# Performance work log

Hardware: AMD Instinct MI355X
Metric: run time of the kernel (lower is better)

The kernel has to match this reference:

```python
import jax, jax.numpy as jnp
import numpy as np

# Module hyper-parameters (match init_kwargs)
H = 8          # num_heads
F = 32         # attention_filters
HF = H * F     # 256, equals input channels C
RY, RX = 2, 2  # spatial_radius
PH, PW = 2 * RY + 1, 2 * RX + 1
S = PH * PW    # 25 neighbor offsets


def setup_inputs() -> dict:
    key = jax.random.key(0)
    ks = jax.random.split(key, 6)
    B, Y, X, C = 8, 128, 128, 256
    x = jax.random.normal(ks[0], (B, Y, X, C), dtype=jnp.float32)
    sc = 0.02
    Wq = jax.random.normal(ks[1], (C, HF), dtype=jnp.float32) * sc
    Wk = jax.random.normal(ks[2], (C, HF), dtype=jnp.float32) * sc
    Wv = jax.random.normal(ks[3], (C, HF), dtype=jnp.float32) * sc
    Wout = jax.random.normal(ks[4], (HF, C), dtype=jnp.float32) * sc
    pos_emb = jax.random.normal(ks[5], (S, HF), dtype=jnp.float32) * sc
    return {"x": x, "Wq": Wq, "Wk": Wk, "Wv": Wv, "Wout": Wout, "pos_emb": pos_emb}


def _centers(n, r):
    # clipped patch-center coordinate for each position
    c = jnp.arange(n)
    return jnp.clip(c, r, n - r - 1)


def reference(x, Wq, Wk, Wv, Wout, pos_emb):
    B, Y, X, C = x.shape
    dtype = x.dtype
    # 1x1 conv projections == channel matmuls
    Q = jnp.einsum('byxc,cf->byxf', x, Wq)
    K = jnp.einsum('byxc,cf->byxf', x, Wk)
    V = jnp.einsum('byxc,cf->byxf', x, Wv)

    # query spatial positional embedding (relative position to clipped center)
    yc = _centers(Y, RY)
    xc = _centers(X, RX)
    y_rel = jnp.arange(Y) - yc + RY          # [Y]
    x_rel = jnp.arange(X) - xc + RX          # [X]
    q_idx = y_rel[:, None] * PW + x_rel[None, :]  # [Y, X]
    Q = Q + pos_emb[q_idx]                   # [B,Y,X,HF]
    Q = Q.reshape(B, Y, X, H, F)

    scale = jnp.asarray(1.0 / np.sqrt(F), dtype)

    offsets = [(dy, dx) for dy in range(-RY, RY + 1) for dx in range(-RX, RX + 1)]

    # pass 1: per-offset scores (loop over fixed 25-neighborhood, rest vectorized)
    scores = []
    for s_idx, (dy, dx) in enumerate(offsets):
        ny = jnp.clip(yc + dy, 0, Y - 1)     # [Y]
        nx = jnp.clip(xc + dx, 0, X - 1)     # [X]
        Kn = K[:, ny][:, :, nx] + pos_emb[s_idx]        # [B,Y,X,HF]
        Kn = Kn.reshape(B, Y, X, H, F)
        scores.append(jnp.einsum('byxhf,byxhf->byxh', Q, Kn) * scale)
    scores = jnp.stack(scores, axis=-1)      # [B,Y,X,H,S]
    weights = jax.nn.softmax(scores, axis=-1)

    # pass 2: weighted value accumulation
    out_acc = jnp.zeros((B, Y, X, H, F), dtype=dtype)
    for s_idx, (dy, dx) in enumerate(offsets):
        ny = jnp.clip(yc + dy, 0, Y - 1)
        nx = jnp.clip(xc + dx, 0, X - 1)
        Vn = V[:, ny][:, :, nx].reshape(B, Y, X, H, F)
        out_acc = out_acc + weights[..., s_idx, None] * Vn

    out_acc = out_acc.reshape(B, Y, X, HF)
    out = jnp.einsum('byxf,fc->byxc', out_acc, Wout)
    return out
```

## Files before the change

kernel.cpp:

```cpp
#include <hip/hip_runtime.h>

#define DEVI __device__ __forceinline__

typedef short v8s __attribute__((ext_vector_type(8)));
typedef float v4f __attribute__((ext_vector_type(4)));
typedef unsigned short u16;

typedef __attribute__((address_space(3))) unsigned int lds_u32;
typedef const __attribute__((address_space(1))) unsigned int glb_u32;

DEVI float bf2f(short s) {
  union { unsigned u; float f; } cv;
  cv.u = ((unsigned)(u16)s) << 16;
  return cv.f;
}
DEVI short f2bf(float f) {
  union { float f; unsigned u; } cv; cv.f = f;
  unsigned u = cv.u;
  return (short)((u + 0x7FFFu + ((u >> 16) & 1u)) >> 16);
}
DEVI void gld16(const void* g, void* l) {
  __builtin_amdgcn_global_load_lds((glb_u32*)g, (lds_u32*)l, 16, 0, 0);
}

__global__ void prep_weights(const float* __restrict__ Wq, const float* __restrict__ Wk,
                             const float* __restrict__ Wv, const float* __restrict__ Wout,
                             short* __restrict__ WcT, short* __restrict__ WoT) {
  int n = blockIdx.x;
  int k = threadIdx.x;
  float v;
  if (n < 256)      v = Wq[k * 256 + n];
  else if (n < 512) v = Wk[k * 256 + (n - 256)];
  else              v = Wv[k * 256 + (n - 512)];
  WcT[n * 256 + k] = f2bf(v);
  if (n < 256) WoT[n * 256 + k] = f2bf(Wout[k * 256 + n]);
}

__global__ void x_cast(const float* __restrict__ x, short* __restrict__ xb) {
  for (size_t gidx = (size_t)blockIdx.x * 256 + threadIdx.x; gidx < 4194304;
       gidx += (size_t)4096 * 256) {
    const float4* src = reinterpret_cast<const float4*>(x + gidx * 8);
    float4 a = src[0], c = src[1];
    v8s pk;
    pk[0] = f2bf(a.x); pk[1] = f2bf(a.y); pk[2] = f2bf(a.z); pk[3] = f2bf(a.w);
    pk[4] = f2bf(c.x); pk[5] = f2bf(c.y); pk[6] = f2bf(c.z); pk[7] = f2bf(c.w);
    *reinterpret_cast<v8s*>(xb + gidx * 8) = pk;
  }
}

__launch_bounds__(256, 3)
__global__ void proj_gemm(const short* __restrict__ xb, const short* __restrict__ WcT,
                          const float* __restrict__ pos_emb,
                          short* __restrict__ Qb, short* __restrict__ Kb,
                          short* __restrict__ Vb) {
  __shared__ short As[128 * 64];
  __shared__ short Bs[128 * 64];
  const int t = threadIdx.x;
  const int bi = blockIdx.x;
  const int xcd = bi & 7;
  const int j = bi >> 3;
  const int mgl = j / 6, nt = j % 6;
  const int mtg = xcd * 32 + mgl;
  const int m0 = mtg * 512;
  const int n0 = nt * 128;
  const int wave = t >> 6, lane = t & 63;
  const int wm = (wave & 1) * 64, wn = (wave >> 1) * 64;
  const int lr = lane & 15, g = lane >> 4;

  const int ro = lane >> 3;
  const int colb = ((lane & 7) * 16) ^ (ro << 4);
  const char* aSrc0 = reinterpret_cast<const char*>(xb + (size_t)(m0 + ro) * 256) + colb;
  const char* bSrc  = reinterpret_cast<const char*>(WcT + (size_t)(n0 + ro) * 256) + colb;

#pragma unroll 1
  for (int u = 0; u < 4; ++u) {
    const char* aSrc = aSrc0 + (size_t)u * 128 * 512;

    v4f acc[4][4];
#pragma unroll
    for (int i = 0; i < 4; ++i)
#pragma unroll
      for (int jj = 0; jj < 4; ++jj) acc[i][jj] = (v4f){0.f, 0.f, 0.f, 0.f};

#pragma unroll 1
    for (int ks = 0; ks < 4; ++ks) {
      __syncthreads();
#pragma unroll
      for (int c = 0; c < 4; ++c) {
        int cc = wave * 4 + c;
        gld16(aSrc + (size_t)cc * 8 * 512 + ks * 128, (char*)As + cc * 1024);
        gld16(bSrc + (size_t)cc * 8 * 512 + ks * 128, (char*)Bs + cc * 1024);
      }
      __syncthreads();
#pragma unroll
      for (int kk = 0; kk < 2; ++kk) {
        v8s af[4], bfr[4];
#pragma unroll
        for (int i = 0; i < 4; ++i) {
          int row = wm + i * 16 + lr;
          int byte = (row * 128 + kk * 64 + g * 16) ^ ((row & 7) << 4);
          af[i] = *reinterpret_cast<const v8s*>(reinterpret_cast<const char*>(As) + byte);
        }
#pragma unroll
        for (int jj = 0; jj < 4; ++jj) {
          int rn = wn + jj * 16 + lr;
          int byte = (rn * 128 + kk * 64 + g * 16) ^ ((rn & 7) << 4);
          bfr[jj] = *reinterpret_cast<const v8s*>(reinterpret_cast<const char*>(Bs) + byte);
        }
#pragma unroll
        for (int i = 0; i < 4; ++i)
#pragma unroll
          for (int jj = 0; jj < 4; ++jj)
            acc[i][jj] = __builtin_amdgcn_mfma_f32_16x16x32_bf16(af[i], bfr[jj], acc[i][jj], 0, 0, 0);
      }
    }

#pragma unroll
    for (int i = 0; i < 4; ++i) {
#pragma unroll
      for (int jj = 0; jj < 4; ++jj) {
        int colg = n0 + wn + jj * 16 + lr;
#pragma unroll
        for (int r = 0; r < 4; ++r) {
          int p = m0 + u * 128 + wm + i * 16 + g * 4 + r;
          float v = acc[i][jj][r];
          if (nt < 2) {
            int yy = (p >> 7) & 127, xx = p & 127;
            int qi = (yy - min(max(yy, 2), 125) + 2) * 5 + (xx - min(max(xx, 2), 125) + 2);
            v += pos_emb[qi * 256 + colg];
            Qb[(size_t)p * 256 + colg] = f2bf(v);
          } else if (nt < 4) {
            Kb[(size_t)p * 256 + (colg - 256)] = f2bf(v);
          } else {
            Vb[(size_t)p * 256 + (colg - 512)] = f2bf(v);
          }
        }
      }
    }
  }
}

__launch_bounds__(256, 4)
__global__ void attn_kernel(const short* __restrict__ Qb, const short* __restrict__ Kb,
                            const short* __restrict__ Vb, const float* __restrict__ pos_emb,
                            short* __restrict__ ACC) {
  __shared__ float pe[25 * 256];
  for (int i = threadIdx.x; i < 1600; i += 256) {
    float4 vv = reinterpret_cast<const float4*>(pos_emb)[i];
    int w = i * 4;
    int f = w & 255;
    int dst = (w & ~255) + (f ^ ((f >> 5) << 2));
    *reinterpret_cast<float4*>(pe + dst) = vv;
  }

  const int t = threadIdx.x;
  const int half = t & 1, h = (t >> 1) & 7, pl = t >> 4;
  const int id = blockIdx.x;
  const int b = id & 7;
  const int local = id >> 3;
  const int bx = local & 31, by = local >> 5;
  const int xx = bx * 4 + (pl & 3);
  const int yy = by * 4 + (pl >> 2);
  const int yc = min(max(yy, 2), 125), xc = min(max(xx, 2), 125);
  const int fo = h * 32 + half * 16;
  const int hx4 = h << 2;
  const size_t pbase = ((size_t)((b * 128 + yy) * 128 + xx)) * 256 + fo;
  const size_t cbase = ((size_t)((b * 128 + yc) * 128 + xc)) * 256 + fo;
  const float SCALE = 0.17677669529663689f;

  float q[16];
  {
    v8s q0 = *reinterpret_cast<const v8s*>(Qb + pbase);
    v8s q1 = *reinterpret_cast<const v8s*>(Qb + pbase + 8);
#pragma unroll
    for (int e = 0; e < 8; ++e) { q[e] = bf2f(q0[e]); q[8 + e] = bf2f(q1[e]); }
  }
  __syncthreads();

  float l = 0.f;
  float oa[16];
#pragma unroll
  for (int f = 0; f < 16; ++f) oa[f] = 0.f;

  const short* kb = Kb + cbase;
  const short* vb = Vb + cbase;
  const float* pb = pe + h * 32;
  const int j0 = (half * 16) ^ hx4;
  const int j1 = (half * 16 + 4) ^ hx4;
  const int j2 = (half * 16 + 8) ^ hx4;
  const int j3 = (half * 16 + 12) ^ hx4;

#pragma unroll 1
  for (int dy = -2; dy <= 2; ++dy) {
    const short* krow = kb + dy * (128 * 256);
    const short* vrow = vb + dy * (128 * 256);
    const float* prow = pb + ((dy + 2) * 5) * 256;
#pragma unroll 1
    for (int dx = -2; dx <= 2; ++dx) {
      const short* kp = krow + dx * 256;
      const short* vp = vrow + dx * 256;
      const float* pp = prow + (dx + 2) * 256;
      v8s k0 = *reinterpret_cast<const v8s*>(kp);
      v8s k1 = *reinterpret_cast<const v8s*>(kp + 8);
      v8s v0 = *reinterpret_cast<const v8s*>(vp);
      v8s v1 = *reinterpret_cast<const v8s*>(vp + 8);
      float4 p0 = *reinterpret_cast<const float4*>(pp + j0);
      float4 p1 = *reinterpret_cast<const float4*>(pp + j1);
      float4 p2 = *reinterpret_cast<const float4*>(pp + j2);
      float4 p3 = *reinterpret_cast<const float4*>(pp + j3);
      float d0 = 0.f, d1 = 0.f, d2 = 0.f, d3 = 0.f;
#pragma unroll
      for (int e = 0; e < 4; ++e) {
        d0 = fmaf(q[e], bf2f(k0[e]), d0);
        d1 = fmaf(q[4 + e], bf2f(k0[4 + e]), d1);
        d2 = fmaf(q[8 + e], bf2f(k1[e]), d2);
        d3 = fmaf(q[12 + e], bf2f(k1[4 + e]), d3);
      }
      d0 = fmaf(q[0], p0.x, d0); d0 = fmaf(q[1], p0.y, d0);
      d0 = fmaf(q[2], p0.z, d0); d0 = fmaf(q[3], p0.w, d0);
      d1 = fmaf(q[4], p1.x, d1); d1 = fmaf(q[5], p1.y, d1);
      d1 = fmaf(q[6], p1.z, d1); d1 = fmaf(q[7], p1.w, d1);
      d2 = fmaf(q[8], p2.x, d2); d2 = fmaf(q[9], p2.y, d2);
      d2 = fmaf(q[10], p2.z, d2); d2 = fmaf(q[11], p2.w, d2);
      d3 = fmaf(q[12], p3.x, d3); d3 = fmaf(q[13], p3.y, d3);
      d3 = fmaf(q[14], p3.z, d3); d3 = fmaf(q[15], p3.w, d3);
      float part = ((d0 + d1) + (d2 + d3)) * SCALE;
      float full = part + __shfl_xor(part, 1);
      float w = __expf(full);
      l += w;
#pragma unroll
      for (int e = 0; e < 8; ++e) oa[e] = fmaf(w, bf2f(v0[e]), oa[e]);
#pragma unroll
      for (int e = 0; e < 8; ++e) oa[8 + e] = fmaf(w, bf2f(v1[e]), oa[8 + e]);
    }
  }

  float inv = 1.f / l;
  v8s o0, o1;
#pragma unroll
  for (int e = 0; e < 8; ++e) { o0[e] = f2bf(oa[e] * inv); o1[e] = f2bf(oa[8 + e] * inv); }
  *reinterpret_cast<v8s*>(ACC + pbase) = o0;
  *reinterpret_cast<v8s*>(ACC + pbase + 8) = o1;
}

__launch_bounds__(256, 3)
__global__ void out_gemm(const short* __restrict__ A, const short* __restrict__ WoT,
                         float* __restrict__ out) {
  __shared__ short As[128 * 64];
  __shared__ short Bs[128 * 64];
  const int t = threadIdx.x;
  const int bi = blockIdx.x;
  const int xcd = bi & 7;
  const int j = bi >> 3;
  const int mgl = j / 2, nt = j % 2;
  const int mtg = xcd * 64 + mgl;
  const int m0 = mtg * 256;
  const int n0 = nt * 128;
  const int wave = t >> 6, lane = t & 63;
  const int wm = (wave & 1) * 64, wn = (wave >> 1) * 64;
  const int lr = lane & 15, g = lane >> 4;

  const int ro = lane >> 3;
  const int colb = ((lane & 7) * 16) ^ (ro << 4);
  const char* aSrc0 = reinterpret_cast<const char*>(A + (size_t)(m0 + ro) * 256) + colb;
  const char* bSrc  = reinterpret_cast<const char*>(WoT + (size_t)(n0 + ro) * 256) + colb;

#pragma unroll 1
  for (int u = 0; u < 2; ++u) {
    const char* aSrc = aSrc0 + (size_t)u * 128 * 512;

    v4f acc[4][4];
#pragma unroll
    for (int i = 0; i < 4; ++i)
#pragma unroll
      for (int jj = 0; jj < 4; ++jj) acc[i][jj] = (v4f){0.f, 0.f, 0.f, 0.f};

#pragma unroll 1
    for (int ks = 0; ks < 4; ++ks) {
      __syncthreads();
#pragma unroll
      for (int c = 0; c < 4; ++c) {
        int cc = wave * 4 + c;
        gld16(aSrc + (size_t)cc * 8 * 512 + ks * 128, (char*)As + cc * 1024);
        gld16(bSrc + (size_t)cc * 8 * 512 + ks * 128, (char*)Bs + cc * 1024);
      }
      __syncthreads();
#pragma unroll
      for (int kk = 0; kk < 2; ++kk) {
        v8s af[4], bfr[4];
#pragma unroll
        for (int i = 0; i < 4; ++i) {
          int row = wm + i * 16 + lr;
          int byte = (row * 128 + kk * 64 + g * 16) ^ ((row & 7) << 4);
          af[i] = *reinterpret_cast<const v8s*>(reinterpret_cast<const char*>(As) + byte);
        }
#pragma unroll
        for (int jj = 0; jj < 4; ++jj) {
          int rn = wn + jj * 16 + lr;
          int byte = (rn * 128 + kk * 64 + g * 16) ^ ((rn & 7) << 4);
          bfr[jj] = *reinterpret_cast<const v8s*>(reinterpret_cast<const char*>(Bs) + byte);
        }
#pragma unroll
        for (int i = 0; i < 4; ++i)
#pragma unroll
          for (int jj = 0; jj < 4; ++jj)
            acc[i][jj] = __builtin_amdgcn_mfma_f32_16x16x32_bf16(af[i], bfr[jj], acc[i][jj], 0, 0, 0);
      }
    }

#pragma unroll
    for (int i = 0; i < 4; ++i) {
#pragma unroll
      for (int jj = 0; jj < 4; ++jj) {
        int colg = n0 + wn + jj * 16 + lr;
#pragma unroll
        for (int r = 0; r < 4; ++r) {
          int p = m0 + u * 128 + wm + i * 16 + g * 4 + r;
          out[(size_t)p * 256 + colg] = acc[i][jj][r];
        }
      }
    }
  }
}

extern "C" void kernel_launch(void* const* d_in, const int* in_sizes, int n_in,
                              void* d_out, int out_size, void* d_ws, size_t ws_size,
                              hipStream_t stream) {
  const float* x       = (const float*)d_in[0];
  const float* Wq      = (const float*)d_in[1];
  const float* Wk      = (const float*)d_in[2];
  const float* Wv      = (const float*)d_in[3];
  const float* Wout    = (const float*)d_in[4];
  const float* pos_emb = (const float*)d_in[5];
  float* out = (float*)d_out;

  char* ws = (char*)d_ws;
  short* WcT  = (short*)ws;
  short* WoT  = (short*)(ws + 393216);
  short* Qb   = (short*)(ws + 524288);
  short* Kb   = Qb + (size_t)131072 * 256;
  short* Vb   = Kb + (size_t)131072 * 256;
  short* ACCb = Vb + (size_t)131072 * 256;
  short* xb   = ACCb;

  prep_weights<<<768, 256, 0, stream>>>(Wq, Wk, Wv, Wout, WcT, WoT);
  x_cast<<<4096, 256, 0, stream>>>(x, xb);
  proj_gemm<<<1536, 256, 0, stream>>>(xb, WcT, pos_emb, Qb, Kb, Vb);
  attn_kernel<<<8192, 256, 0, stream>>>(Qb, Kb, Vb, pos_emb, ACCb);
  out_gemm<<<1024, 256, 0, stream>>>(ACCb, WoT, out);
}
```

Baseline: 377.5 us.

## Double-buffer LDS tiles in projection and output GEMMs to overlap loads

Both GEMM kernels now use two LDS buffers and issue the next K-step's global-to-LDS loads before computing the current one. The u/ks nested loops are flattened into one stage loop, with epilogue stores every fourth step and manual vmcnt waits plus barriers. This hides global load latency behind MFMA work. In exchange, LDS per block doubles and launch bounds drop from 3 to 2 blocks per CU, which lowers occupancy. Stores at the end of each tile also sit inside the pipelined loop.

```diff
diff --git a/kernel.cpp b/kernel.cpp
--- a/kernel.cpp
+++ b/kernel.cpp
@@ -48,13 +48,13 @@
   }
 }
 
-__launch_bounds__(256, 3)
+__launch_bounds__(256, 2)
 __global__ void proj_gemm(const short* __restrict__ xb, const short* __restrict__ WcT,
                           const float* __restrict__ pos_emb,
                           short* __restrict__ Qb, short* __restrict__ Kb,
                           short* __restrict__ Vb) {
-  __shared__ short As[128 * 64];
-  __shared__ short Bs[128 * 64];
+  __shared__ short As[2][128 * 64];
+  __shared__ short Bs[2][128 * 64];
   const int t = threadIdx.x;
   const int bi = blockIdx.x;
   const int xcd = bi & 7;
@@ -70,73 +70,92 @@
   const int ro = lane >> 3;
   const int colb = ((lane & 7) * 16) ^ (ro << 4);
   const char* aSrc0 = reinterpret_cast<const char*>(xb + (size_t)(m0 + ro) * 256) + colb;
-  const char* bSrc  = reinterpret_cast<const char*>(WcT + (size_t)(n0 + ro) * 256) + colb;
-
+  const char* bSrc0 = reinterpret_cast<const char*>(WcT + (size_t)(n0 + ro) * 256) + colb;
+
+  v4f acc[4][4];
+#pragma unroll
+  for (int i = 0; i < 4; ++i)
+#pragma unroll
+    for (int jj = 0; jj < 4; ++jj) acc[i][jj] = (v4f){0.f, 0.f, 0.f, 0.f};
+
+  auto stage = [&](int buf, int s) {
+    const int u = s >> 2, ks = s & 3;
+    const char* aS = aSrc0 + (size_t)u * 128 * 512 + ks * 128;
+    const char* bS = bSrc0 + ks * 128;
+    char* aD = (char*)As + buf * 16384;
+    char* bD = (char*)Bs + buf * 16384;
+#pragma unroll
+    for (int c = 0; c < 4; ++c) {
+      int cc = wave * 4 + c;
+      gld16(aS + (size_t)cc * 8 * 512, aD + cc * 1024);
+      gld16(bS + (size_t)cc * 8 * 512, bD + cc * 1024);
+    }
+  };
+
+  stage(0, 0);
 #pragma unroll 1
-  for (int u = 0; u < 4; ++u) {
-    const char* aSrc = aSrc0 + (size_t)u * 128 * 512;
-
-    v4f acc[4][4];
-#pragma unroll
-    for (int i = 0; i < 4; ++i)
-#pragma unroll
-      for (int jj = 0; jj < 4; ++jj) acc[i][jj] = (v4f){0.f, 0.f, 0.f, 0.f};
-
-#pragma unroll 1
-    for (int ks = 0; ks < 4; ++ks) {
-      __syncthreads();
-#pragma unroll
-      for (int c = 0; c < 4; ++c) {
-        int cc = wave * 4 + c;
-        gld16(aSrc + (size_t)cc * 8 * 512 + ks * 128, (char*)As + cc * 1024);
-        gld16(bSrc + (size_t)cc * 8 * 512 + ks * 128, (char*)Bs + cc * 1024);
-      }
-      __syncthreads();
-#pragma unroll
-      for (int kk = 0; kk < 2; ++kk) {
-        v8s af[4], bfr[4];
-#pragma unroll
-        for (int i = 0; i < 4; ++i) {
-          int row = wm + i * 16 + lr;
-          int byte = (row * 128 + kk * 64 + g * 16) ^ ((row & 7) << 4);
-          af[i] = *reinterpret_cast<const v8s*>(reinterpret_cast<const char*>(As) + byte);
-        }
+  for (int s = 0; s < 16; ++s) {
+    const int buf = s & 1;
+    if (s < 15) {
+      stage(buf ^ 1, s + 1);
+      asm volatile("s_waitcnt vmcnt(8)" ::: "memory");
+    } else {
+      asm volatile("s_waitcnt vmcnt(0)" ::: "memory");
+    }
+    __builtin_amdgcn_s_barrier();
+    __builtin_amdgcn_sched_barrier(0);
+
+    const char* aB = (const char*)As + buf * 16384;
+    const char* bB = (const char*)Bs + buf * 16384;
+#pragma unroll
+    for (int kk = 0; kk < 2; ++kk) {
+      v8s af[4], bfr[4];
+#pragma unroll
+      for (int i = 0; i < 4; ++i) {
+        int row = wm + i * 16 + lr;
+        int byte = (row * 128 + kk * 64 + g * 16) ^ ((row & 7) << 4);
+        af[i] = *reinterpret_cast<const v8s*>(aB + byte);
+      }
+#pragma unroll
+      for (int jj = 0; jj < 4; ++jj) {
+        int rn = wn + jj * 16 + lr;
+        int byte = (rn * 128 + kk * 64 + g * 16) ^ ((rn & 7) << 4);
+        bfr[jj] = *reinterpret_cast<const v8s*>(bB + byte);
+      }
+#pragma unroll
+      for (int i = 0; i < 4; ++i)
+#pragma unroll
+        for (int jj = 0; jj < 4; ++jj)
+          acc[i][jj] = __builtin_amdgcn_mfma_f32_16x16x32_bf16(af[i], bfr[jj], acc[i][jj], 0, 0, 0);
+    }
+
+    if ((s & 3) == 3) {
+      const int u = s >> 2;
+#pragma unroll
+      for (int i = 0; i < 4; ++i) {
 #pragma unroll
         for (int jj = 0; jj < 4; ++jj) {
-          int rn = wn + jj * 16 + lr;
-          int byte = (rn * 128 + kk * 64 + g * 16) ^ ((rn & 7) << 4);
-          bfr[jj] = *reinterpret_cast<const v8s*>(reinterpret_cast<const char*>(Bs) + byte);
-        }
-#pragma unroll
-        for (int i = 0; i < 4; ++i)
-#pragma unroll
-          for (int jj = 0; jj < 4; ++jj)
-            acc[i][jj] = __builtin_amdgcn_mfma_f32_16x16x32_bf16(af[i], bfr[jj], acc[i][jj], 0, 0, 0);
-      }
-    }
-
-#pragma unroll
-    for (int i = 0; i < 4; ++i) {
-#pragma unroll
-      for (int jj = 0; jj < 4; ++jj) {
-        int colg = n0 + wn + jj * 16 + lr;
-#pragma unroll
-        for (int r = 0; r < 4; ++r) {
-          int p = m0 + u * 128 + wm + i * 16 + g * 4 + r;
-          float v = acc[i][jj][r];
-          if (nt < 2) {
-            int yy = (p >> 7) & 127, xx = p & 127;
-            int qi = (yy - min(max(yy, 2), 125) + 2) * 5 + (xx - min(max(xx, 2), 125) + 2);
-            v += pos_emb[qi * 256 + colg];
-            Qb[(size_t)p * 256 + colg] = f2bf(v);
-          } else if (nt < 4) {
-            Kb[(size_t)p * 256 + (colg - 256)] = f2bf(v);
-          } else {
-            Vb[(size_t)p * 256 + (colg - 512)] = f2bf(v);
+          int colg = n0 + wn + jj * 16 + lr;
+#pragma unroll
+          for (int r = 0; r < 4; ++r) {
+            int p = m0 + u * 128 + wm + i * 16 + g * 4 + r;
+            float v = acc[i][jj][r];
+            if (nt < 2) {
+              int yy = (p >> 7) & 127, xx = p & 127;
+              int qi = (yy - min(max(yy, 2), 125) + 2) * 5 + (xx - min(max(xx, 2), 125) + 2);
+              v += pos_emb[qi * 256 + colg];
+              Qb[(size_t)p * 256 + colg] = f2bf(v);
+            } else if (nt < 4) {
+              Kb[(size_t)p * 256 + (colg - 256)] = f2bf(v);
+            } else {
+              Vb[(size_t)p * 256 + (colg - 512)] = f2bf(v);
+            }
+            acc[i][jj][r] = 0.f;
           }
         }
       }
     }
+    __builtin_amdgcn_s_barrier();
   }
 }
 
@@ -243,11 +262,11 @@
   *reinterpret_cast<v8s*>(ACC + pbase + 8) = o1;
 }
 
-__launch_bounds__(256, 3)
+__launch_bounds__(256, 2)
 __global__ void out_gemm(const short* __restrict__ A, const short* __restrict__ WoT,
                          float* __restrict__ out) {
-  __shared__ short As[128 * 64];
-  __shared__ short Bs[128 * 64];
+  __shared__ short As[2][128 * 64];
+  __shared__ short Bs[2][128 * 64];
   const int t = threadIdx.x;
   const int bi = blockIdx.x;
   const int xcd = bi & 7;
@@ -263,63 +282,82 @@
   const int ro = lane >> 3;
   const int colb = ((lane & 7) * 16) ^ (ro << 4);
   const char* aSrc0 = reinterpret_cast<const char*>(A + (size_t)(m0 + ro) * 256) + colb;
-  const char* bSrc  = reinterpret_cast<const char*>(WoT + (size_t)(n0 + ro) * 256) + colb;
-
+  const char* bSrc0 = reinterpret_cast<const char*>(WoT + (size_t)(n0 + ro) * 256) + colb;
+
+  v4f acc[4][4];
+#pragma unroll
+  for (int i = 0; i < 4; ++i)
+#pragma unroll
+    for (int jj = 0; jj < 4; ++jj) acc[i][jj] = (v4f){0.f, 0.f, 0.f, 0.f};
+
+  auto stage = [&](int buf, int s) {
+    const int u = s >> 2, ks = s & 3;
+    const char* aS = aSrc0 + (size_t)u * 128 * 512 + ks * 128;
+    const char* bS = bSrc0 + ks * 128;
+    char* aD = (char*)As + buf * 16384;
+    char* bD = (char*)Bs + buf * 16384;
+#pragma unroll
+    for (int c = 0; c < 4; ++c) {
+      int cc = wave * 4 + c;
+      gld16(aS + (size_t)cc * 8 * 512, aD + cc * 1024);
+      gld16(bS + (size_t)cc * 8 * 512, bD + cc * 1024);
+    }
+  };
+
+  stage(0, 0);
 #pragma unroll 1
-  for (int u = 0; u < 2; ++u) {
-    const char* aSrc = aSrc0 + (size_t)u * 128 * 512;
-
-    v4f acc[4][4];
-#pragma unroll
-    for (int i = 0; i < 4; ++i)
-#pragma unroll
-      for (int jj = 0; jj < 4; ++jj) acc[i][jj] = (v4f){0.f, 0.f, 0.f, 0.f};
-
-#pragma unroll 1
-    for (int ks = 0; ks < 4; ++ks) {
-      __syncthreads();
-#pragma unroll
-      for (int c = 0; c < 4; ++c) {
-        int cc = wave * 4 + c;
-        gld16(aSrc + (size_t)cc * 8 * 512 + ks * 128, (char*)As + cc * 1024);
-        gld16(bSrc + (size_t)cc * 8 * 512 + ks * 128, (char*)Bs + cc * 1024);
-      }
-      __syncthreads();
-#pragma unroll
-      for (int kk = 0; kk < 2; ++kk) {
-        v8s af[4], bfr[4];
-#pragma unroll
-        for (int i = 0; i < 4; ++i) {
-          int row = wm + i * 16 + lr;
-          int byte = (row * 128 + kk * 64 + g * 16) ^ ((row & 7) << 4);
-          af[i] = *reinterpret_cast<const v8s*>(reinterpret_cast<const char*>(As) + byte);
+  for (int s = 0; s < 8; ++s) {
+    const int buf = s & 1;
+    if (s < 7) {
+      stage(buf ^ 1, s + 1);
+      asm volatile("s_waitcnt vmcnt(8)" ::: "memory");
+    } else {
+      asm volatile("s_waitcnt vmcnt(0)" ::: "memory");
+    }
+    __builtin_amdgcn_s_barrier();
+    __builtin_amdgcn_sched_barrier(0);
+
+    const char* aB = (const char*)As + buf * 16384;
+    const char* bB = (const char*)Bs + buf * 16384;
+#pragma unroll
+    for (int kk = 0; kk < 2; ++kk) {
+      v8s af[4], bfr[4];
+#pragma unroll
+      for (int i = 0; i < 4; ++i) {
+        int row = wm + i * 16 + lr;
+        int byte = (row * 128 + kk * 64 + g * 16) ^ ((row & 7) << 4);
+        af[i] = *reinterpret_cast<const v8s*>(aB + byte);
+      }
+#pragma unroll
+      for (int jj = 0; jj < 4; ++jj) {
+        int rn = wn + jj * 16 + lr;
+        int byte = (rn * 128 + kk * 64 + g * 16) ^ ((rn & 7) << 4);
+        bfr[jj] = *reinterpret_cast<const v8s*>(bB + byte);
+      }
+#pragma unroll
+      for (int i = 0; i < 4; ++i)
+#pragma unroll
+        for (int jj = 0; jj < 4; ++jj)
+          acc[i][jj] = __builtin_amdgcn_mfma_f32_16x16x32_bf16(af[i], bfr[jj], acc[i][jj], 0, 0, 0);
+    }
+
+    if ((s & 3) == 3) {
+      const int u = s >> 2;
+#pragma unroll
+      for (int i = 0; i < 4; ++i) {
+#pragma unroll
+        for (int jj = 0; jj < 4; ++jj) {
+          int colg = n0 + wn + jj * 16 + lr;
+#pragma unroll
+          for (int r = 0; r < 4; ++r) {
+            int p = m0 + u * 128 + wm + i * 16 + g * 4 + r;
+            out[(size_t)p * 256 + colg] = acc[i][jj][r];
+            acc[i][jj][r] = 0.f;
+          }
         }
-#pragma unroll
-        for (int jj = 0; jj < 4; ++jj) {
-          int rn = wn + jj * 16 + lr;
-          int byte = (rn * 128 + kk * 64 + g * 16) ^ ((rn & 7) << 4);
-          bfr[jj] = *reinterpret_cast<const v8s*>(reinterpret_cast<const char*>(Bs) + byte);
-        }
-#pragma unroll
-        for (int i = 0; i < 4; ++i)
-#pragma unroll
-          for (int jj = 0; jj < 4; ++jj)
-            acc[i][jj] = __builtin_amdgcn_mfma_f32_16x16x32_bf16(af[i], bfr[jj], acc[i][jj], 0, 0, 0);
-      }
-    }
-
-#pragma unroll
-    for (int i = 0; i < 4; ++i) {
-#pragma unroll
-      for (int jj = 0; jj < 4; ++jj) {
-        int colg = n0 + wn + jj * 16 + lr;
-#pragma unroll
-        for (int r = 0; r < 4; ++r) {
-          int p = m0 + u * 128 + wm + i * 16 + g * 4 + r;
-          out[(size_t)p * 256 + colg] = acc[i][jj][r];
-        }
-      }
-    }
+      }
+    }
+    __builtin_amdgcn_s_barrier();
   }
 }
 
```

Result: slower. 409.4 us (+8.4%).

## Triple-buffer projection GEMM loads and stage epilogue through LDS for vector stores

Applied to the files above, without the earlier changes.

Restructures the QKV projection GEMM into one flattened 32-step loop with a triple-buffered LDS ring, using BK=32 slices. Global-to-LDS loads are issued two steps ahead, with explicit vmcnt waits and raw barriers in place of __syncthreads. The epilogue now writes accumulators as bf16 into LDS, then reads them back row-contiguous and emits 16-byte vector stores, adding pos_emb for Q in that pass. This aims to hide load latency and replace scattered 2-byte global stores with coalesced ones. The cost is more barriers and an extra bf16 rounding of Q before the pos_emb add.

```diff
diff --git a/kernel.cpp b/kernel.cpp
--- a/kernel.cpp
+++ b/kernel.cpp
@@ -22,6 +22,9 @@
 DEVI void gld16(const void* g, void* l) {
   __builtin_amdgcn_global_load_lds((glb_u32*)g, (lds_u32*)l, 16, 0, 0);
 }
+#define SBAR() __builtin_amdgcn_s_barrier()
+#define SCHED0() __builtin_amdgcn_sched_barrier(0)
+#define LGKM0() asm volatile("s_waitcnt lgkmcnt(0)" ::: "memory")
 
 __global__ void prep_weights(const float* __restrict__ Wq, const float* __restrict__ Wk,
                              const float* __restrict__ Wv, const float* __restrict__ Wout,
@@ -53,8 +56,7 @@
                           const float* __restrict__ pos_emb,
                           short* __restrict__ Qb, short* __restrict__ Kb,
                           short* __restrict__ Vb) {
-  __shared__ short As[128 * 64];
-  __shared__ short Bs[128 * 64];
+  __shared__ short L[3][8192];
   const int t = threadIdx.x;
   const int bi = blockIdx.x;
   const int xcd = bi & 7;
@@ -67,76 +69,121 @@
   const int wm = (wave & 1) * 64, wn = (wave >> 1) * 64;
   const int lr = lane & 15, g = lane >> 4;
 
-  const int ro = lane >> 3;
-  const int colb = ((lane & 7) * 16) ^ (ro << 4);
-  const char* aSrc0 = reinterpret_cast<const char*>(xb + (size_t)(m0 + ro) * 256) + colb;
-  const char* bSrc  = reinterpret_cast<const char*>(WcT + (size_t)(n0 + ro) * 256) + colb;
-
-#pragma unroll 1
-  for (int u = 0; u < 4; ++u) {
-    const char* aSrc = aSrc0 + (size_t)u * 128 * 512;
-
-    v4f acc[4][4];
+  const int srow = wave * 16 + (lane >> 2);
+  const int scu = (lane & 3) ^ ((lane >> 2) & 3);
+  const char* aSrcBase = reinterpret_cast<const char*>(xb) + (size_t)(m0 + srow) * 512 + scu * 16;
+  const char* bSrcBase = reinterpret_cast<const char*>(WcT) + (size_t)(n0 + srow) * 512 + scu * 16;
+
+  v4f acc[4][4];
+#pragma unroll
+  for (int i = 0; i < 4; ++i)
+#pragma unroll
+    for (int jj = 0; jj < 4; ++jj) acc[i][jj] = (v4f){0.f, 0.f, 0.f, 0.f};
+
+  auto stage = [&](int buf, int s) {
+    const int um = s >> 3, ks = s & 7;
+    const char* aS = aSrcBase + (size_t)um * 65536 + ks * 64;
+    const char* bS = bSrcBase + ks * 64;
+    char* aD = (char*)&L[buf][0] + wave * 1024;
+    char* bD = (char*)&L[buf][4096] + wave * 1024;
+    gld16(aS, aD);
+    gld16(aS + 32768, aD + 4096);
+    gld16(bS, bD);
+    gld16(bS + 32768, bD + 4096);
+  };
+
+  stage(0, 0);
+  stage(1, 1);
+
+#pragma unroll 1
+  for (int s = 0; s < 32; ++s) {
+    const int buf = s % 3;
+    if (s < 30) stage((s + 2) % 3, s + 2);
+    if (s >= 30) {
+      if (s == 30) asm volatile("s_waitcnt vmcnt(4)" ::: "memory");
+      else         asm volatile("s_waitcnt vmcnt(0)" ::: "memory");
+    } else if (s > 0 && (s & 7) == 0) {
+      if (nt < 2) asm volatile("s_waitcnt vmcnt(32)" ::: "memory");
+      else        asm volatile("s_waitcnt vmcnt(16)" ::: "memory");
+    } else {
+      asm volatile("s_waitcnt vmcnt(8)" ::: "memory");
+    }
+    SBAR();
+    SCHED0();
+
+    const char* aB = (const char*)&L[buf][0];
+    const char* bB = (const char*)&L[buf][4096];
+    v8s af[4], bfr[4];
+#pragma unroll
+    for (int i = 0; i < 4; ++i) {
+      int row = wm + i * 16 + lr;
+      af[i] = *reinterpret_cast<const v8s*>(aB + row * 64 + ((g * 16) ^ ((row & 3) << 4)));
+    }
+#pragma unroll
+    for (int jj = 0; jj < 4; ++jj) {
+      int rn = wn + jj * 16 + lr;
+      bfr[jj] = *reinterpret_cast<const v8s*>(bB + rn * 64 + ((g * 16) ^ ((rn & 3) << 4)));
+    }
 #pragma unroll
     for (int i = 0; i < 4; ++i)
 #pragma unroll
-      for (int jj = 0; jj < 4; ++jj) acc[i][jj] = (v4f){0.f, 0.f, 0.f, 0.f};
-
-#pragma unroll 1
-    for (int ks = 0; ks < 4; ++ks) {
-      __syncthreads();
-#pragma unroll
-      for (int c = 0; c < 4; ++c) {
-        int cc = wave * 4 + c;
-        gld16(aSrc + (size_t)cc * 8 * 512 + ks * 128, (char*)As + cc * 1024);
-        gld16(bSrc + (size_t)cc * 8 * 512 + ks * 128, (char*)Bs + cc * 1024);
-      }
-      __syncthreads();
-#pragma unroll
-      for (int kk = 0; kk < 2; ++kk) {
-        v8s af[4], bfr[4];
-#pragma unroll
-        for (int i = 0; i < 4; ++i) {
-          int row = wm + i * 16 + lr;
-          int byte = (row * 128 + kk * 64 + g * 16) ^ ((row & 7) << 4);
-          af[i] = *reinterpret_cast<const v8s*>(reinterpret_cast<const char*>(As) + byte);
-        }
-#pragma unroll
-        for (int jj = 0; jj < 4; ++jj) {
-          int rn = wn + jj * 16 + lr;
-          int byte = (rn * 128 + kk * 64 + g * 16) ^ ((rn & 7) << 4);
-          bfr[jj] = *reinterpret_cast<const v8s*>(reinterpret_cast<const char*>(Bs) + byte);
-        }
-#pragma unroll
-        for (int i = 0; i < 4; ++i)
-#pragma unroll
-          for (int jj = 0; jj < 4; ++jj)
-            acc[i][jj] = __builtin_amdgcn_mfma_f32_16x16x32_bf16(af[i], bfr[jj], acc[i][jj], 0, 0, 0);
-      }
-    }
-
-#pragma unroll
-    for (int i = 0; i < 4; ++i) {
-#pragma unroll
-      for (int jj = 0; jj < 4; ++jj) {
-        int colg = n0 + wn + jj * 16 + lr;
-#pragma unroll
-        for (int r = 0; r < 4; ++r) {
-          int p = m0 + u * 128 + wm + i * 16 + g * 4 + r;
-          float v = acc[i][jj][r];
+      for (int jj = 0; jj < 4; ++jj)
+        acc[i][jj] = __builtin_amdgcn_mfma_f32_16x16x32_bf16(af[i], bfr[jj], acc[i][jj], 0, 0, 0);
+
+    if ((s & 7) == 7) {
+      const int um = s >> 3;
+      char* tb = (char*)&L[buf][0];
+#pragma unroll 1
+      for (int pass = 0; pass < 2; ++pass) {
+        LGKM0(); SBAR(); SCHED0();
+        if (wm == pass * 64) {
+#pragma unroll
+          for (int i = 0; i < 4; ++i)
+#pragma unroll
+            for (int jj = 0; jj < 4; ++jj)
+#pragma unroll
+              for (int r = 0; r < 4; ++r) {
+                int rowl = i * 16 + g * 4 + r;
+                int col = wn + jj * 16 + lr;
+                int byte = (rowl * 256 + col * 2) ^ ((rowl & 7) << 4);
+                *reinterpret_cast<short*>(tb + byte) = f2bf(acc[i][jj][r]);
+              }
+        }
+        LGKM0(); SBAR(); SCHED0();
+        {
+          int row = t >> 2, seg = t & 3;
+          int prow = m0 + um * 128 + pass * 64 + row;
+          v8s vals[4];
+#pragma unroll
+          for (int q = 0; q < 4; ++q)
+            vals[q] = *reinterpret_cast<const v8s*>(
+                tb + ((row * 256 + seg * 64 + q * 16) ^ ((row & 7) << 4)));
           if (nt < 2) {
-            int yy = (p >> 7) & 127, xx = p & 127;
+            int yy = (prow >> 7) & 127, xx = prow & 127;
             int qi = (yy - min(max(yy, 2), 125) + 2) * 5 + (xx - min(max(xx, 2), 125) + 2);
-            v += pos_emb[qi * 256 + colg];
-            Qb[(size_t)p * 256 + colg] = f2bf(v);
-          } else if (nt < 4) {
-            Kb[(size_t)p * 256 + (colg - 256)] = f2bf(v);
+            const float* peb = pos_emb + qi * 256 + n0 + seg * 32;
+#pragma unroll
+            for (int q = 0; q < 4; ++q) {
+              v8s v = vals[q];
+#pragma unroll
+              for (int e = 0; e < 8; ++e) v[e] = f2bf(bf2f(v[e]) + peb[q * 8 + e]);
+              *reinterpret_cast<v8s*>(Qb + (size_t)prow * 256 + n0 + seg * 32 + q * 8) = v;
+            }
           } else {
-            Vb[(size_t)p * 256 + (colg - 512)] = f2bf(v);
+            short* dst = (nt < 4) ? Kb : Vb;
+            const int colb = n0 + seg * 32 - ((nt < 4) ? 256 : 512);
+#pragma unroll
+            for (int q = 0; q < 4; ++q)
+              *reinterpret_cast<v8s*>(dst + (size_t)prow * 256 + colb + q * 8) = vals[q];
           }
         }
       }
-    }
+#pragma unroll
+      for (int i = 0; i < 4; ++i)
+#pragma unroll
+        for (int jj = 0; jj < 4; ++jj) acc[i][jj] = (v4f){0.f, 0.f, 0.f, 0.f};
+    }
+    if (s < 31) { LGKM0(); SBAR(); SCHED0(); }
   }
 }
 
```

New measurement: 560.8 us. +48.5%, slower.

## Keep weight tile resident in LDS and double-buffer activation chunks in projection GEMM

Applied to the files above, without the earlier changes.

The projection GEMM now loads its full 128x256 weight slice into LDS once per block and keeps it there. Activation chunks of 64 rows by the full K=256 are double-buffered, so the next chunk's global-to-LDS copy is issued before the current chunk's MFMAs, with explicit vmcnt waits and raw barriers in place of syncthreads. The aim is to overlap memory traffic with compute and cut per-K-step barrier stalls. In exchange, LDS use grows to about 128KB per block, which forces occupancy down to one block per CU.

```diff
diff --git a/kernel.cpp b/kernel.cpp
--- a/kernel.cpp
+++ b/kernel.cpp
@@ -22,6 +22,8 @@
 DEVI void gld16(const void* g, void* l) {
   __builtin_amdgcn_global_load_lds((glb_u32*)g, (lds_u32*)l, 16, 0, 0);
 }
+#define SBAR() __builtin_amdgcn_s_barrier()
+#define SCHED0() __builtin_amdgcn_sched_barrier(0)
 
 __global__ void prep_weights(const float* __restrict__ Wq, const float* __restrict__ Wk,
                              const float* __restrict__ Wv, const float* __restrict__ Wout,
@@ -48,81 +50,95 @@
   }
 }
 
-__launch_bounds__(256, 3)
+__launch_bounds__(256, 1)
 __global__ void proj_gemm(const short* __restrict__ xb, const short* __restrict__ WcT,
                           const float* __restrict__ pos_emb,
                           short* __restrict__ Qb, short* __restrict__ Kb,
                           short* __restrict__ Vb) {
-  __shared__ short As[128 * 64];
-  __shared__ short Bs[128 * 64];
+  __shared__ short Bres[128 * 256];
+  __shared__ short Ach[2][64 * 256];
   const int t = threadIdx.x;
   const int bi = blockIdx.x;
   const int xcd = bi & 7;
   const int j = bi >> 3;
   const int mgl = j / 6, nt = j % 6;
-  const int mtg = xcd * 32 + mgl;
-  const int m0 = mtg * 512;
+  const int mg = xcd * 32 + mgl;
   const int n0 = nt * 128;
   const int wave = t >> 6, lane = t & 63;
-  const int wm = (wave & 1) * 64, wn = (wave >> 1) * 64;
+  const int wm = (wave & 1) * 32, wn = (wave >> 1) * 64;
   const int lr = lane & 15, g = lane >> 4;
 
-  const int ro = lane >> 3;
-  const int colb = ((lane & 7) * 16) ^ (ro << 4);
-  const char* aSrc0 = reinterpret_cast<const char*>(xb + (size_t)(m0 + ro) * 256) + colb;
-  const char* bSrc  = reinterpret_cast<const char*>(WcT + (size_t)(n0 + ro) * 256) + colb;
-
-#pragma unroll 1
-  for (int u = 0; u < 4; ++u) {
-    const char* aSrc = aSrc0 + (size_t)u * 128 * 512;
-
-    v4f acc[4][4];
-#pragma unroll
-    for (int i = 0; i < 4; ++i)
-#pragma unroll
-      for (int jj = 0; jj < 4; ++jj) acc[i][jj] = (v4f){0.f, 0.f, 0.f, 0.f};
-
-#pragma unroll 1
-    for (int ks = 0; ks < 4; ++ks) {
-      __syncthreads();
-#pragma unroll
-      for (int c = 0; c < 4; ++c) {
-        int cc = wave * 4 + c;
-        gld16(aSrc + (size_t)cc * 8 * 512 + ks * 128, (char*)As + cc * 1024);
-        gld16(bSrc + (size_t)cc * 8 * 512 + ks * 128, (char*)Bs + cc * 1024);
-      }
-      __syncthreads();
-#pragma unroll
-      for (int kk = 0; kk < 2; ++kk) {
-        v8s af[4], bfr[4];
-#pragma unroll
-        for (int i = 0; i < 4; ++i) {
-          int row = wm + i * 16 + lr;
-          int byte = (row * 128 + kk * 64 + g * 16) ^ ((row & 7) << 4);
-          af[i] = *reinterpret_cast<const v8s*>(reinterpret_cast<const char*>(As) + byte);
-        }
-#pragma unroll
-        for (int jj = 0; jj < 4; ++jj) {
-          int rn = wn + jj * 16 + lr;
-          int byte = (rn * 128 + kk * 64 + g * 16) ^ ((rn & 7) << 4);
-          bfr[jj] = *reinterpret_cast<const v8s*>(reinterpret_cast<const char*>(Bs) + byte);
-        }
-#pragma unroll
-        for (int i = 0; i < 4; ++i)
-#pragma unroll
-          for (int jj = 0; jj < 4; ++jj)
-            acc[i][jj] = __builtin_amdgcn_mfma_f32_16x16x32_bf16(af[i], bfr[jj], acc[i][jj], 0, 0, 0);
-      }
-    }
-
-#pragma unroll
-    for (int i = 0; i < 4; ++i) {
+  const int rl = wave * 2 + (lane >> 5);
+  const int cl = (lane & 31) ^ (rl & 7);
+
+  {
+    const char* bsrc = reinterpret_cast<const char*>(WcT + (size_t)n0 * 256)
+                       + rl * 512 + cl * 16;
+    char* bdst = (char*)Bres + wave * 1024;
+#pragma unroll
+    for (int i = 0; i < 16; ++i)
+      gld16(bsrc + (size_t)i * 4096, bdst + i * 4096);
+  }
+  const char* asrc0 = reinterpret_cast<const char*>(xb)
+                      + (size_t)mg * 8 * 32768 + rl * 512 + cl * 16;
+
+  auto stageA = [&](int buf, int k) {
+    const char* s = asrc0 + (size_t)k * 32768;
+    char* d = (char*)Ach[buf] + wave * 1024;
+#pragma unroll
+    for (int i = 0; i < 8; ++i)
+      gld16(s + (size_t)i * 4096, d + i * 4096);
+  };
+
+  v4f acc[2][4];
+#pragma unroll
+  for (int i = 0; i < 2; ++i)
+#pragma unroll
+    for (int jj = 0; jj < 4; ++jj) acc[i][jj] = (v4f){0.f, 0.f, 0.f, 0.f};
+
+  stageA(0, 0);
+  asm volatile("s_waitcnt vmcnt(0)" ::: "memory");
+  SBAR();
+  SCHED0();
+
+#pragma unroll 1
+  for (int k = 0; k < 8; ++k) {
+    const int cur = k & 1;
+    if (k < 7) stageA(cur ^ 1, k + 1);
+
+    const char* aB = (const char*)Ach[cur];
+    const char* bB = (const char*)Bres;
+#pragma unroll
+    for (int ks = 0; ks < 8; ++ks) {
+      v8s af[2], bfr[4];
+#pragma unroll
+      for (int i = 0; i < 2; ++i) {
+        int row = wm + i * 16 + lr;
+        af[i] = *reinterpret_cast<const v8s*>(
+            aB + row * 512 + (((ks * 4 + g) ^ (row & 7)) << 4));
+      }
+#pragma unroll
+      for (int jj = 0; jj < 4; ++jj) {
+        int rn = wn + jj * 16 + lr;
+        bfr[jj] = *reinterpret_cast<const v8s*>(
+            bB + rn * 512 + (((ks * 4 + g) ^ (rn & 7)) << 4));
+      }
+#pragma unroll
+      for (int i = 0; i < 2; ++i)
+#pragma unroll
+        for (int jj = 0; jj < 4; ++jj)
+          acc[i][jj] = __builtin_amdgcn_mfma_f32_16x16x32_bf16(af[i], bfr[jj], acc[i][jj], 0, 0, 0);
+    }
+
+    const int prow0 = (mg * 8 + k) * 64;
+#pragma unroll
+    for (int i = 0; i < 2; ++i) {
 #pragma unroll
       for (int jj = 0; jj < 4; ++jj) {
         int colg = n0 + wn + jj * 16 + lr;
 #pragma unroll
         for (int r = 0; r < 4; ++r) {
-          int p = m0 + u * 128 + wm + i * 16 + g * 4 + r;
+          int p = prow0 + wm + i * 16 + g * 4 + r;
           float v = acc[i][jj][r];
           if (nt < 2) {
             int yy = (p >> 7) & 127, xx = p & 127;
@@ -134,9 +150,15 @@
           } else {
             Vb[(size_t)p * 256 + (colg - 512)] = f2bf(v);
           }
+          acc[i][jj][r] = 0.f;
         }
       }
     }
+
+    if (k < 7) asm volatile("s_waitcnt vmcnt(32)" ::: "memory");
+    else       asm volatile("s_waitcnt vmcnt(0)" ::: "memory");
+    SBAR();
+    SCHED0();
   }
 }
 
```

Measured after the change: 469.7 us. 1.24x slower.
